# Kernel optimization log

Measured on AMD Instinct MI355X. Metric: run time of the kernel, lower is better.

The kernel has to match this reference:

```python
import math
import jax, jax.numpy as jnp
import numpy as np

B, S, D = 4, 2048, 1024
H, HD = 16, 64
NUM_BUCKETS = 32
MAX_DISTANCE = 128
EPS = 1e-6
ENC_S = 512


def _relative_position_bucket(relative_position):
    # bidirectional=False path
    num_buckets = NUM_BUCKETS
    rp = -jnp.minimum(relative_position, 0)  # [S, S] nonneg
    max_exact = num_buckets // 2
    is_small = rp < max_exact
    scale = (num_buckets - max_exact) / math.log(MAX_DISTANCE / max_exact)
    large = max_exact + (jnp.log(jnp.maximum(rp, 1).astype(jnp.float32) / max_exact) * scale).astype(jnp.int32)
    large = jnp.minimum(large, num_buckets - 1)
    return jnp.where(is_small, rp, large)


def compute_bias(rel_emb, q_len, k_len):
    ctx = jnp.arange(q_len)[:, None]
    mem = jnp.arange(k_len)[None, :]
    bucket = _relative_position_bucket(mem - ctx)          # [q, k] int
    values = rel_emb[bucket]                                # [q, k, H]
    return jnp.transpose(values, (2, 0, 1))[None]           # [1, H, q, k]


def setup_inputs() -> dict:
    key = jax.random.key(0)
    ks = jax.random.split(key, 8)
    std = 0.02
    return {
        "input_ids": jax.random.normal(ks[0], (B, S, D), jnp.float32),
        "encoder_output": jax.random.normal(ks[1], (B, ENC_S, D), jnp.float32),
        "wq": jax.random.normal(ks[2], (D, H * HD), jnp.float32) * std,
        "wk": jax.random.normal(ks[3], (D, H * HD), jnp.float32) * std,
        "wv": jax.random.normal(ks[4], (D, H * HD), jnp.float32) * std,
        "wo": jax.random.normal(ks[5], (H * HD, D), jnp.float32) * std,
        "rel_emb": jax.random.normal(ks[6], (NUM_BUCKETS, H), jnp.float32) * std,
        "ln_w": jnp.ones((D,), jnp.float32),
    }


def reference(input_ids, encoder_output, wq, wk, wv, wo, rel_emb, ln_w):
    origin = input_ids
    # MT5LayerNorm: RMS norm, no mean subtraction, no bias
    variance = jnp.mean(jnp.square(input_ids.astype(jnp.float32)), axis=-1, keepdims=True)
    x = (input_ids * jax.lax.rsqrt(variance + EPS)) * ln_w

    q = (x @ wq).reshape(B, S, H, HD)
    k = (x @ wk).reshape(B, S, H, HD)
    v = (x @ wv).reshape(B, S, H, HD)

    # NOTE: T5-style attention has no 1/sqrt(d) scaling
    scores = jnp.einsum("bqhd,bkhd->bhqk", q, k)
    scores = scores + compute_bias(rel_emb, S, S)
    attn = jax.nn.softmax(scores, axis=-1)
    ctx = jnp.einsum("bhqk,bkhd->bqhd", attn, v).reshape(B, S, H * HD)
    attn_out = ctx @ wo

    # residual connection (dropout is identity at rate 0 / eval)
    return origin + attn_out
```

## Files before the change

kernel.cpp:

```cpp
#include <hip/hip_runtime.h>
#include <hip/hip_bf16.h>
#include <math.h>

#define S_LEN 2048
#define D_DIM 1024
#define NHEAD 16

typedef __attribute__((ext_vector_type(8))) short bf16x8;
typedef __attribute__((ext_vector_type(4))) float floatx4;

__device__ __forceinline__ short f32_bf16(float f) {
  union { float f; unsigned u; } v; v.f = f;
  unsigned r = v.u + 0x7FFFu + ((v.u >> 16) & 1u);
  return (short)(r >> 16);
}

__device__ __forceinline__ float exp2_fast(float x) {
#if __has_builtin(__builtin_amdgcn_exp2f)
  return __builtin_amdgcn_exp2f(x);
#else
  float r; asm("v_exp_f32 %0, %1" : "=v"(r) : "v"(x)); return r;
#endif
}

__device__ __forceinline__ void gload16(const void* g, void* l) {
  __builtin_amdgcn_global_load_lds((const __attribute__((address_space(1))) unsigned*)g,
                                   (__attribute__((address_space(3))) unsigned*)l,
                                   16, 0, 0);
}

__global__ __launch_bounds__(256) void rmsnorm_k(const float* __restrict__ x,
                                                 const float* __restrict__ w,
                                                 short* __restrict__ out) {
  int row = blockIdx.x;
  const float4* xr = (const float4*)(x + (size_t)row * D_DIM);
  float4 v = xr[threadIdx.x];
  float ss = v.x*v.x + v.y*v.y + v.z*v.z + v.w*v.w;
  #pragma unroll
  for (int off = 32; off > 0; off >>= 1) ss += __shfl_xor(ss, off);
  __shared__ float red[4];
  if ((threadIdx.x & 63) == 0) red[threadIdx.x >> 6] = ss;
  __syncthreads();
  float scale = rsqrtf((red[0]+red[1]+red[2]+red[3]) * (1.f/D_DIM) + 1e-6f);
  float4 wv = ((const float4*)w)[threadIdx.x];
  short4 o;
  o.x = f32_bf16(v.x*scale*wv.x);
  o.y = f32_bf16(v.y*scale*wv.y);
  o.z = f32_bf16(v.z*scale*wv.z);
  o.w = f32_bf16(v.w*scale*wv.w);
  ((short4*)out)[(size_t)row*256 + threadIdx.x] = o;
}

__global__ __launch_bounds__(256) void pack_wqkv_k(const float* __restrict__ wq,
                                                   const float* __restrict__ wk,
                                                   const float* __restrict__ wv,
                                                   short* __restrict__ o) {
  int t = blockIdx.x*256 + threadIdx.x;
  int n = t >> 10, k = t & 1023;
  const float* src = (n < 1024) ? wq : ((n < 2048) ? wk : wv);
  float scale = (n < 1024) ? 1.44269504f : 1.0f;
  o[t] = f32_bf16(src[(size_t)k*1024 + (n & 1023)] * scale);
}

__global__ __launch_bounds__(256) void pack_wo_k(const float* __restrict__ wo,
                                                 short* __restrict__ o) {
  int t = blockIdx.x*256 + threadIdx.x;
  int n = t >> 10, k = t & 1023;
  o[t] = f32_bf16(wo[(size_t)k*1024 + n]);
}

template<bool ADD_RES>
__global__ __launch_bounds__(256) void gemm_bt(const short* __restrict__ A,
                                               const short* __restrict__ Bt,
                                               short* __restrict__ Cb,
                                               float* __restrict__ Cf,
                                               const float* __restrict__ res,
                                               int M, int N, int K) {
  constexpr int BK = 64;
  __shared__ __align__(16) short As[128*BK];
  __shared__ __align__(16) short Bs[128*BK];
  int tid = threadIdx.x;
  int w = tid >> 6, lane = tid & 63, quad = lane >> 4, l16 = lane & 15;
  int wr = w >> 1, wc = w & 1;
  int bn = blockIdx.x, bm = blockIdx.y;
  const short* Ag = A + (size_t)bm * 128 * K;
  const short* Bg = Bt + (size_t)bn * 128 * K;
  const int srow = lane >> 3;
  const int slc  = (lane & 7) ^ srow;

  floatx4 acc[4][4] = {};

  for (int k0 = 0; k0 < K; k0 += BK) {
    #pragma unroll
    for (int i = 0; i < 4; i++) {
      int rbase = w*32 + i*8;
      gload16(Ag + (size_t)(rbase + srow) * K + k0 + slc*8, &As[rbase*BK]);
      gload16(Bg + (size_t)(rbase + srow) * K + k0 + slc*8, &Bs[rbase*BK]);
    }
    __syncthreads();
    #pragma unroll
    for (int h = 0; h < 2; h++) {
      int sw = ((quad + 4*h) ^ (l16 & 7)) * 8;
      bf16x8 af[4], bfr[4];
      #pragma unroll
      for (int i = 0; i < 4; i++) {
        af[i]  = *(const bf16x8*)&As[(wr*64 + i*16 + l16)*BK + sw];
        bfr[i] = *(const bf16x8*)&Bs[(wc*64 + i*16 + l16)*BK + sw];
      }
      #pragma unroll
      for (int i = 0; i < 4; i++)
        #pragma unroll
        for (int j = 0; j < 4; j++)
          acc[i][j] = __builtin_amdgcn_mfma_f32_16x16x32_bf16(af[i], bfr[j], acc[i][j], 0, 0, 0);
    }
    __syncthreads();
  }

  #pragma unroll
  for (int i = 0; i < 4; i++) {
    int row0 = bm*128 + wr*64 + i*16 + quad*4;
    #pragma unroll
    for (int j = 0; j < 4; j++) {
      int col = bn*128 + wc*64 + j*16 + l16;
      #pragma unroll
      for (int r = 0; r < 4; r++) {
        size_t idx = (size_t)(row0 + r) * N + col;
        if (ADD_RES) Cf[idx] = res[idx] + acc[i][j][r];
        else         Cb[idx] = f32_bf16(acc[i][j][r]);
      }
    }
  }
}

__global__ __launch_bounds__(256) void pack_vt_k(const short* __restrict__ qkv,
                                                 short* __restrict__ vt) {
  __shared__ __align__(16) short tile[64][72];
  int s0 = blockIdx.x * 64;
  int bh = blockIdx.y;
  int b = bh >> 4, h = bh & 15;
  int t = threadIdx.x;
  #pragma unroll
  for (int i = 0; i < 2; i++) {
    int idx = t + i*256;
    int s = idx >> 3, c = idx & 7;
    *(bf16x8*)&tile[s][c*8] =
      *(const bf16x8*)&qkv[(size_t)(b*S_LEN + s0 + s)*3072 + 2048 + h*64 + c*8];
  }
  __syncthreads();
  #pragma unroll
  for (int i = 0; i < 2; i++) {
    int idx = t + i*256;
    int hd = idx >> 3, c = idx & 7;
    short tmp[8];
    #pragma unroll
    for (int j = 0; j < 8; j++) tmp[j] = tile[c*8 + j][hd];
    *(bf16x8*)&vt[((size_t)(bh*64 + hd))*S_LEN + s0 + c*8] = *(bf16x8*)tmp;
  }
}

__global__ __launch_bounds__(512) void flash_k(const short* __restrict__ qkv,
                                               const short* __restrict__ vt,
                                               const float* __restrict__ rel_emb,
                                               short* __restrict__ ctx) {
  __shared__ __align__(16) short Kb[2][64*64];
  __shared__ __align__(16) short Vb[2][64*64];
  __shared__ float lut2[132];

  const int L = blockIdx.x + 8*blockIdx.y;
  const int xcd = L & 7, kk_ = L >> 3;
  const int bh = xcd*8 + (kk_ >> 3);
  const int qt = kk_ & 7;
  const int b = bh >> 4, h = bh & 15;
  const int t = threadIdx.x, w = t >> 6, lane = t & 63, quad = lane >> 4, l16 = lane & 15;
  const float L2E = 1.44269504f;

  if (t < 129) {
    int rp = t, bucket;
    if (rp < 16) bucket = rp;
    else {
      bucket = 16 + (int)(logf((float)rp * 0.0625f) * (16.f / logf(8.f)));
      if (bucket > 31) bucket = 31;
    }
    lut2[t] = rel_emb[bucket*16 + h] * L2E;
  }
  const float bfut  = rel_emb[h] * L2E;
  const float bpast = rel_emb[31*16 + h] * L2E;
  const floatx4 bf4 = {bfut, bfut, bfut, bfut};
  const floatx4 bp4 = {bpast, bpast, bpast, bpast};
  const floatx4 zz4 = {0.f, 0.f, 0.f, 0.f};

  const int srow = lane >> 3;
  const int slc  = (lane & 7) ^ srow;
  const int rho  = w*8 + srow;
  const int kperm = 32*(rho >> 5) + 8*((rho >> 2) & 3) + 4*((rho >> 4) & 1) + (rho & 3);

  const short* kgU = qkv + ((size_t)b*S_LEN)*3072 + 1024 + h*64;
  const int    loK = kperm*3072 + slc*8;
  const short* vgU = vt + ((size_t)bh*64)*2048;
  const int    loV = rho*2048 + slc*8;

  bf16x8 qB[2][2];
  #pragma unroll
  for (int rb = 0; rb < 2; rb++) {
    const short* qb = qkv + ((size_t)(b*S_LEN + qt*256 + rb*128 + w*16 + l16))*3072 + h*64;
    qB[rb][0] = *(const bf16x8*)&qb[quad*8];
    qB[rb][1] = *(const bf16x8*)&qb[32 + quad*8];
  }

  floatx4 o[2][4] = {};
  floatx4 li4[2] = {};
  const short ONE = (short)0x3F80;
  bf16x8 onesA = {ONE, ONE, ONE, ONE, ONE, ONE, ONE, ONE};

  const int swz0 = (quad     ^ (l16 & 7)) * 8;
  const int swz1 = ((quad+4) ^ (l16 & 7)) * 8;

  #define STAGE(P_, KT_) do {                                                   \
    const short* ka_ = kgU + (size_t)(KT_)*196608 + loK;                        \
    gload16(ka_, &Kb[P_][(w*8)*64]);                                            \
    const short* va_ = vgU + loV + (KT_)*64;                                    \
    gload16(va_, &Vb[P_][(w*8)*64]);                                            \
  } while (0)

  #define BODY(P_, KT_) do {                                                    \
    __syncthreads();                                                            \
    if ((KT_) < 31) STAGE((P_) ^ 1, (KT_) + 1);      \
    bool boundary = ((KT_) >= 4*qt - 2) && ((KT_) <= 4*qt + 3);                 \
    floatx4 cinit = boundary ? zz4 : (((KT_) >= 4*qt) ? bf4 : bp4);             \
    floatx4 sc[2][4];                                                           \
    _Pragma("unroll")                                                           \
    for (int c = 0; c < 4; c++) {                                               \
      int rowA = (c*16 + l16)*64;                                               \
      bf16x8 ka0 = *(const bf16x8*)&Kb[P_][rowA + swz0];                        \
      bf16x8 ka1 = *(const bf16x8*)&Kb[P_][rowA + swz1];                        \
      _Pragma("unroll")                                                         \
      for (int rb = 0; rb < 2; rb++) {                                          \
        floatx4 z = __builtin_amdgcn_mfma_f32_16x16x32_bf16(ka0, qB[rb][0], cinit, 0, 0, 0); \
        z = __builtin_amdgcn_mfma_f32_16x16x32_bf16(ka1, qB[rb][1], z, 0, 0, 0);\
        sc[rb][c] = z;                                                          \
      }                                                                         \
    }                                                                           \
    if (boundary) {                                                             \
      _Pragma("unroll")                                                         \
      for (int rb = 0; rb < 2; rb++) {                                          \
        int q0 = qt*256 + rb*128 + w*16 + l16;                                  \
        _Pragma("unroll")                                                       \
        for (int c = 0; c < 4; c++) {                                           \
          int kk = (KT_)*64 + 32*(c >> 1) + 8*quad + 4*(c & 1);                 \
          _Pragma("unroll")                                                     \
          for (int r = 0; r < 4; r++) {                                         \
            int d = q0 - (kk + r);                                              \
            d = d < 0 ? 0 : (d > 128 ? 128 : d);                                \
            sc[rb][c][r] += lut2[d];                                            \
          }                                                                     \
        }                                                                       \
      }                                                                         \
    }                                                                           \
    _Pragma("unroll")                                                           \
    for (int rb = 0; rb < 2; rb++)                                              \
      _Pragma("unroll")                                                         \
      for (int c = 0; c < 4; c++)                                               \
        _Pragma("unroll")                                                       \
        for (int r = 0; r < 4; r++)                                             \
          sc[rb][c][r] = exp2_fast(sc[rb][c][r]);                               \
    bf16x8 pf[2][2];                                                            \
    _Pragma("unroll")                                                           \
    for (int rb = 0; rb < 2; rb++) {                                            \
      _Pragma("unroll")                                                         \
      for (int hh = 0; hh < 2; hh++) {                                          \
        union { bf16x8 v; unsigned u[4]; } pk;                                  \
        floatx4 a = sc[rb][2*hh], bb = sc[rb][2*hh + 1];                        \
        pk.u[0] = __builtin_amdgcn_perm(__float_as_uint(a[1]),  __float_as_uint(a[0]),  0x07060302); \
        pk.u[1] = __builtin_amdgcn_perm(__float_as_uint(a[3]),  __float_as_uint(a[2]),  0x07060302); \
        pk.u[2] = __builtin_amdgcn_perm(__float_as_uint(bb[1]), __float_as_uint(bb[0]), 0x07060302); \
        pk.u[3] = __builtin_amdgcn_perm(__float_as_uint(bb[3]), __float_as_uint(bb[2]), 0x07060302); \
        pf[rb][hh] = pk.v;                                                      \
      }                                                                         \
    }                                                                           \
    _Pragma("unroll")                                                           \
    for (int rb = 0; rb < 2; rb++) {                                            \
      li4[rb] = __builtin_amdgcn_mfma_f32_16x16x32_bf16(onesA, pf[rb][0], li4[rb], 0, 0, 0); \
      li4[rb] = __builtin_amdgcn_mfma_f32_16x16x32_bf16(onesA, pf[rb][1], li4[rb], 0, 0, 0); \
    }                                                                           \
    _Pragma("unroll")                                                           \
    for (int jj = 0; jj < 4; jj++) {                                            \
      int rowV = (jj*16 + l16)*64;                                              \
      bf16x8 va0 = *(const bf16x8*)&Vb[P_][rowV + swz0];                        \
      bf16x8 va1 = *(const bf16x8*)&Vb[P_][rowV + swz1];                        \
      _Pragma("unroll")                                                         \
      for (int rb = 0; rb < 2; rb++) {                                          \
        o[rb][jj] = __builtin_amdgcn_mfma_f32_16x16x32_bf16(va0, pf[rb][0], o[rb][jj], 0, 0, 0); \
        o[rb][jj] = __builtin_amdgcn_mfma_f32_16x16x32_bf16(va1, pf[rb][1], o[rb][jj], 0, 0, 0); \
      }                                                                         \
    }                                                                           \
  } while (0)

  STAGE(0, 0);
  for (int kt = 0; kt < 32; kt += 2) {
    BODY(0, kt);
    BODY(1, kt + 1);
  }

  #pragma unroll
  for (int rb = 0; rb < 2; rb++) {
    float inv = 1.f / li4[rb][0];
    size_t row = (size_t)(b*S_LEN + qt*256 + rb*128 + w*16 + l16);
    #pragma unroll
    for (int jj = 0; jj < 4; jj++) {
      short4 st;
      st.x = f32_bf16(o[rb][jj][0] * inv);
      st.y = f32_bf16(o[rb][jj][1] * inv);
      st.z = f32_bf16(o[rb][jj][2] * inv);
      st.w = f32_bf16(o[rb][jj][3] * inv);
      *(short4*)&ctx[row*1024 + h*64 + jj*16 + quad*4] = st;
    }
  }
  #undef STAGE
  #undef BODY
}

extern "C" void kernel_launch(void* const* d_in, const int* in_sizes, int n_in,
                              void* d_out, int out_size, void* d_ws, size_t ws_size,
                              hipStream_t stream) {
  const float* input_ids = (const float*)d_in[0];
  const float* wq      = (const float*)d_in[2];
  const float* wk      = (const float*)d_in[3];
  const float* wv      = (const float*)d_in[4];
  const float* wo      = (const float*)d_in[5];
  const float* rel_emb = (const float*)d_in[6];
  const float* ln_w    = (const float*)d_in[7];
  float* out = (float*)d_out;

  char* ws = (char*)d_ws;
  short* xb     = (short*)ws;  ws += (size_t)8192*1024*2;
  short* wqkv_t = (short*)ws;  ws += (size_t)3072*1024*2;
  short* wo_t   = (short*)ws;  ws += (size_t)1024*1024*2;
  short* qkv    = (short*)ws;  ws += (size_t)8192*3072*2;
  short* vt     = (short*)ws;  ws += (size_t)64*64*2048*2;
  short* ctx    = (short*)ws;  ws += (size_t)8192*1024*2;

  rmsnorm_k<<<8192, 256, 0, stream>>>(input_ids, ln_w, xb);
  pack_wqkv_k<<<(3072*1024)/256, 256, 0, stream>>>(wq, wk, wv, wqkv_t);
  pack_wo_k<<<(1024*1024)/256, 256, 0, stream>>>(wo, wo_t);
  gemm_bt<false><<<dim3(24, 64), 256, 0, stream>>>(xb, wqkv_t, qkv, nullptr, nullptr,
                                                   8192, 3072, 1024);
  pack_vt_k<<<dim3(32, 64), 256, 0, stream>>>(qkv, vt);
  flash_k<<<dim3(8, 64), 512, 0, stream>>>(qkv, vt, rel_emb, ctx);
  gemm_bt<true><<<dim3(8, 64), 256, 0, stream>>>(ctx, wo_t, nullptr, out, input_ids,
                                                 8192, 1024, 1024);
}
```

Before: 298.1 us.

## Double-buffer GEMM LDS tiles with BK=32 and merge weight pack kernels

The bf16 GEMM now uses two LDS buffers with a K-step of 32. The next tile's global-to-LDS load is issued before the MFMAs on the current tile, leaving one barrier per iteration instead of two, and the swizzle is changed to match the narrower tile. The two weight-packing kernels are merged into one launch to save launch overhead. The smaller K-step doubles the loop iterations and barriers per K, which may offset some of the overlap gained.

Result: no change. 292.3 us (-1.9%).

```diff
diff --git a/kernel.cpp b/kernel.cpp
--- a/kernel.cpp
+++ b/kernel.cpp
@@ -51,22 +51,23 @@
   ((short4*)out)[(size_t)row*256 + threadIdx.x] = o;
 }
 
-__global__ __launch_bounds__(256) void pack_wqkv_k(const float* __restrict__ wq,
-                                                   const float* __restrict__ wk,
-                                                   const float* __restrict__ wv,
-                                                   short* __restrict__ o) {
+__global__ __launch_bounds__(256) void pack_w_k(const float* __restrict__ wq,
+                                                const float* __restrict__ wk,
+                                                const float* __restrict__ wv,
+                                                const float* __restrict__ wo,
+                                                short* __restrict__ oqkv,
+                                                short* __restrict__ owo) {
   int t = blockIdx.x*256 + threadIdx.x;
-  int n = t >> 10, k = t & 1023;
-  const float* src = (n < 1024) ? wq : ((n < 2048) ? wk : wv);
-  float scale = (n < 1024) ? 1.44269504f : 1.0f;
-  o[t] = f32_bf16(src[(size_t)k*1024 + (n & 1023)] * scale);
-}
-
-__global__ __launch_bounds__(256) void pack_wo_k(const float* __restrict__ wo,
-                                                 short* __restrict__ o) {
-  int t = blockIdx.x*256 + threadIdx.x;
-  int n = t >> 10, k = t & 1023;
-  o[t] = f32_bf16(wo[(size_t)k*1024 + n]);
+  if (t < 3072*1024) {
+    int n = t >> 10, k = t & 1023;
+    const float* src = (n < 1024) ? wq : ((n < 2048) ? wk : wv);
+    float scale = (n < 1024) ? 1.44269504f : 1.0f;
+    oqkv[t] = f32_bf16(src[(size_t)k*1024 + (n & 1023)] * scale);
+  } else {
+    int t2 = t - 3072*1024;
+    int n = t2 >> 10, k = t2 & 1023;
+    owo[t2] = f32_bf16(wo[(size_t)k*1024 + n]);
+  }
 }
 
 template<bool ADD_RES>
@@ -76,45 +77,50 @@
                                                float* __restrict__ Cf,
                                                const float* __restrict__ res,
                                                int M, int N, int K) {
-  constexpr int BK = 64;
-  __shared__ __align__(16) short As[128*BK];
-  __shared__ __align__(16) short Bs[128*BK];
+  constexpr int BK = 32;
+  __shared__ __align__(16) short As[2][128*BK];
+  __shared__ __align__(16) short Bs[2][128*BK];
   int tid = threadIdx.x;
   int w = tid >> 6, lane = tid & 63, quad = lane >> 4, l16 = lane & 15;
   int wr = w >> 1, wc = w & 1;
   int bn = blockIdx.x, bm = blockIdx.y;
   const short* Ag = A + (size_t)bm * 128 * K;
   const short* Bg = Bt + (size_t)bn * 128 * K;
-  const int srow = lane >> 3;
-  const int slc  = (lane & 7) ^ srow;
+  const int r4 = lane >> 2;
+  const int c4 = lane & 3;
+  const int lc = c4 ^ (r4 & 3);
+  const int swz = (quad ^ (l16 & 3)) * 8;
 
   floatx4 acc[4][4] = {};
 
+  #define GSTAGE(p_, k0_) do {                                                  \
+    _Pragma("unroll")                                                           \
+    for (int i = 0; i < 2; i++) {                                               \
+      int c = w + i*4;                                                          \
+      gload16(Ag + (size_t)(c*16 + r4) * K + (k0_) + lc*8, &As[p_][c*16*BK]);   \
+      gload16(Bg + (size_t)(c*16 + r4) * K + (k0_) + lc*8, &Bs[p_][c*16*BK]);   \
+    }                                                                           \
+  } while (0)
+
+  GSTAGE(0, 0);
+  int p = 0;
   for (int k0 = 0; k0 < K; k0 += BK) {
+    __syncthreads();
+    if (k0 + BK < K) GSTAGE(p ^ 1, k0 + BK);
+    bf16x8 af[4], bfr[4];
     #pragma unroll
     for (int i = 0; i < 4; i++) {
-      int rbase = w*32 + i*8;
-      gload16(Ag + (size_t)(rbase + srow) * K + k0 + slc*8, &As[rbase*BK]);
-      gload16(Bg + (size_t)(rbase + srow) * K + k0 + slc*8, &Bs[rbase*BK]);
+      af[i]  = *(const bf16x8*)&As[p][(wr*64 + i*16 + l16)*BK + swz];
+      bfr[i] = *(const bf16x8*)&Bs[p][(wc*64 + i*16 + l16)*BK + swz];
     }
-    __syncthreads();
-    #pragma unroll
-    for (int h = 0; h < 2; h++) {
-      int sw = ((quad + 4*h) ^ (l16 & 7)) * 8;
-      bf16x8 af[4], bfr[4];
+    #pragma unroll
+    for (int i = 0; i < 4; i++)
       #pragma unroll
-      for (int i = 0; i < 4; i++) {
-        af[i]  = *(const bf16x8*)&As[(wr*64 + i*16 + l16)*BK + sw];
-        bfr[i] = *(const bf16x8*)&Bs[(wc*64 + i*16 + l16)*BK + sw];
-      }
-      #pragma unroll
-      for (int i = 0; i < 4; i++)
-        #pragma unroll
-        for (int j = 0; j < 4; j++)
-          acc[i][j] = __builtin_amdgcn_mfma_f32_16x16x32_bf16(af[i], bfr[j], acc[i][j], 0, 0, 0);
-    }
-    __syncthreads();
-  }
+      for (int j = 0; j < 4; j++)
+        acc[i][j] = __builtin_amdgcn_mfma_f32_16x16x32_bf16(af[i], bfr[j], acc[i][j], 0, 0, 0);
+    p ^= 1;
+  }
+  #undef GSTAGE
 
   #pragma unroll
   for (int i = 0; i < 4; i++) {
@@ -340,8 +346,7 @@
   short* ctx    = (short*)ws;  ws += (size_t)8192*1024*2;
 
   rmsnorm_k<<<8192, 256, 0, stream>>>(input_ids, ln_w, xb);
-  pack_wqkv_k<<<(3072*1024)/256, 256, 0, stream>>>(wq, wk, wv, wqkv_t);
-  pack_wo_k<<<(1024*1024)/256, 256, 0, stream>>>(wo, wo_t);
+  pack_w_k<<<16384, 256, 0, stream>>>(wq, wk, wv, wo, wqkv_t, wo_t);
   gemm_bt<false><<<dim3(24, 64), 256, 0, stream>>>(xb, wqkv_t, qkv, nullptr, nullptr,
                                                    8192, 3072, 1024);
   pack_vt_k<<<dim3(32, 64), 256, 0, stream>>>(qkv, vt);
```
